# Performance work log

Hardware: AMD Instinct MI355X
Metric: run time of the kernel (lower is better)

The kernel has to match this reference:

```python
import jax, jax.numpy as jnp
import numpy as np
from jax import lax

D_MODEL = 1024
EXPAND = 2
D_INNER = EXPAND * D_MODEL          # 2048
HEADDIM = 64
NHEADS = D_INNER // HEADDIM         # 32
D_STATE = 128
D_CONV = 4
NGROUPS = 1
CONV_DIM = D_INNER + 2 * NGROUPS * D_STATE            # 2304
D_IN_PROJ = 2 * D_INNER + 2 * NGROUPS * D_STATE + NHEADS  # 4384
BATCH, SEQLEN = 2, 2048
EPS = 1e-5


def setup_inputs() -> dict:
    key = jax.random.key(0)
    ks = jax.random.split(key, 10)
    u = jax.random.normal(ks[0], (BATCH, SEQLEN, D_MODEL), jnp.float32)
    W_in = jax.random.normal(ks[1], (D_IN_PROJ, D_MODEL), jnp.float32) * (D_MODEL ** -0.5)
    conv_w = jax.random.normal(ks[2], (CONV_DIM, D_CONV), jnp.float32) * (D_CONV ** -0.5)
    conv_b = jnp.zeros((CONV_DIM,), jnp.float32)
    dt_bias = jnp.log(jnp.exp(jax.random.uniform(ks[3], (NHEADS,), jnp.float32,
                                                 minval=0.001, maxval=0.1)) - 1.0)
    A_log = jnp.log(jax.random.uniform(ks[4], (NHEADS,), jnp.float32, minval=1.0, maxval=16.0))
    D = jnp.ones((NHEADS,), jnp.float32)
    norm_w = jnp.ones((D_INNER,), jnp.float32)
    W_out = jax.random.normal(ks[5], (D_MODEL, D_INNER), jnp.float32) * (D_INNER ** -0.5)
    return {"u": u, "W_in": W_in, "conv_w": conv_w, "conv_b": conv_b,
            "dt_bias": dt_bias, "A_log": A_log, "D": D, "norm_w": norm_w, "W_out": W_out}


def _causal_depthwise_conv(x, w, b):
    # x: [B, L, C], w: [C, K], b: [C]; causal (left) padding K-1
    K = w.shape[1]
    xp = jnp.pad(x, ((0, 0), (K - 1, 0), (0, 0)))
    L = x.shape[1]
    out = b[None, None, :]
    for k in range(K):  # small fixed loop over taps
        out = out + xp[:, k:k + L, :] * w[:, k][None, None, :]
    return out


def _ssd_scan(dt, A, x, Bm, Cm):
    # dt: [B,L,H], A: [H], x: [B,L,H,P], Bm/Cm: [B,L,N]
    Bsz = x.shape[0]
    dA = jnp.exp(dt * A[None, None, :])          # [B,L,H]
    dtx = dt[..., None] * x                       # [B,L,H,P]

    def step(h, inp):
        dA_t, dtx_t, B_t, C_t = inp               # [B,H],[B,H,P],[B,N],[B,N]
        h = h * dA_t[:, :, None, None] + dtx_t[..., None] * B_t[:, None, None, :]
        y = jnp.einsum('bhpn,bn->bhp', h, C_t)
        return h, y

    h0 = jnp.zeros((Bsz, NHEADS, HEADDIM, D_STATE), x.dtype)
    _, ys = lax.scan(step, h0,
                     (dA.transpose(1, 0, 2), dtx.transpose(1, 0, 2, 3),
                      Bm.transpose(1, 0, 2), Cm.transpose(1, 0, 2)))
    return ys.transpose(1, 0, 2, 3)               # [B,L,H,P]


def reference(u, W_in, conv_w, conv_b, dt_bias, A_log, D, norm_w, W_out):
    Bsz, L, _ = u.shape
    zxbcdt = jnp.einsum('bld,ed->ble', u, W_in)                   # [B,L,D_IN_PROJ]
    z = zxbcdt[..., :D_INNER]
    xBC = zxbcdt[..., D_INNER:D_INNER + CONV_DIM]
    dt = zxbcdt[..., D_INNER + CONV_DIM:]                          # [B,L,H]

    xBC = jax.nn.silu(_causal_depthwise_conv(xBC, conv_w, conv_b))
    x = xBC[..., :D_INNER].reshape(Bsz, L, NHEADS, HEADDIM)
    Bm = xBC[..., D_INNER:D_INNER + D_STATE]                       # ngroups=1 -> [B,L,N]
    Cm = xBC[..., D_INNER + D_STATE:]

    dt = jax.nn.softplus(dt + dt_bias[None, None, :])              # [B,L,H]
    A = -jnp.exp(A_log)                                            # [H]

    y = _ssd_scan(dt, A, x, Bm, Cm)                                # [B,L,H,P]
    y = y + D[None, None, :, None] * x
    y = y.reshape(Bsz, L, D_INNER)

    # gated RMSNorm: rmsnorm(y * silu(z)) * weight
    y = y * jax.nn.silu(z)
    y = y * lax.rsqrt(jnp.mean(y * y, axis=-1, keepdims=True) + EPS) * norm_w[None, None, :]

    return jnp.einsum('ble,de->bld', y, W_out)                     # [B,L,D_MODEL]
```

## Files before the change

### kernel.cpp

```cpp
#include <hip/hip_runtime.h>
#include <hip/hip_bf16.h>
#include <math.h>
#include <stdint.h>

#define D_MODEL   1024
#define D_INNER   2048
#define HEADDIM   64
#define NHEADS    32
#define D_STATE   128
#define D_CONV    4
#define CONV_DIM  (D_INNER + 2 * D_STATE)
#define D_IN_PROJ (2 * D_INNER + 2 * D_STATE + NHEADS)
#define N_PAD     4480
#define BATCH     2
#define SEQLEN    2048
#define BL        (BATCH * SEQLEN)
#define EPS       1e-5f

#define NC    16
#define CHUNK 128

typedef __bf16 bf16x8 __attribute__((ext_vector_type(8)));
typedef float  f32x4  __attribute__((ext_vector_type(4)));
typedef unsigned short u16x8 __attribute__((ext_vector_type(8)));

__device__ __forceinline__ float siluf(float x) {
    return x / (1.0f + expf(-x));
}
__device__ __forceinline__ float softplusf(float x) {
    return (x > 20.0f) ? x : log1pf(expf(x));
}
__device__ __forceinline__ unsigned short f2bf(float f) {
    union { float f; unsigned u; } v; v.f = f;
    unsigned r = (v.u + 0x7FFFu + ((v.u >> 16) & 1u)) >> 16;
    return (unsigned short)r;
}

__global__ __launch_bounds__(256) void cast_bf16_kernel(
    const float* __restrict__ in, unsigned short* __restrict__ out, int n8)
{
    const int i = blockIdx.x * 256 + threadIdx.x;
    if (i >= n8) return;
    const float4* p = reinterpret_cast<const float4*>(in + (size_t)i * 8);
    float4 a = p[0], b = p[1];
    u16x8 o;
    o[0] = f2bf(a.x); o[1] = f2bf(a.y); o[2] = f2bf(a.z); o[3] = f2bf(a.w);
    o[4] = f2bf(b.x); o[5] = f2bf(b.y); o[6] = f2bf(b.z); o[7] = f2bf(b.w);
    *reinterpret_cast<u16x8*>(out + (size_t)i * 8) = o;
}

__global__ __launch_bounds__(256) void cast_win_kernel(
    const float* __restrict__ W, unsigned short* __restrict__ out)
{
    const int i = blockIdx.x * 256 + threadIdx.x;
    if (i >= N_PAD * D_MODEL / 8) return;
    const int row = i / (D_MODEL / 8);
    u16x8 o;
    if (row < D_IN_PROJ) {
        const float4* p = reinterpret_cast<const float4*>(W + (size_t)i * 8);
        float4 a = p[0], b = p[1];
        o[0] = f2bf(a.x); o[1] = f2bf(a.y); o[2] = f2bf(a.z); o[3] = f2bf(a.w);
        o[4] = f2bf(b.x); o[5] = f2bf(b.y); o[6] = f2bf(b.z); o[7] = f2bf(b.w);
    } else {
        o = (u16x8)(unsigned short)0;
    }
    *reinterpret_cast<u16x8*>(out + (size_t)i * 8) = o;
}

#define GBM 128
#define GBK 32

__device__ __forceinline__ unsigned swz(unsigned o) {
    return o ^ (((o >> 7) & 7u) << 4);
}

__device__ __forceinline__ void gld_lds16(const unsigned short* gsrc,
                                          unsigned short* lds) {
    auto* l = reinterpret_cast<__attribute__((address_space(3))) unsigned int*>(
        reinterpret_cast<uintptr_t>(lds));
    const auto* g =
        reinterpret_cast<const __attribute__((address_space(1))) unsigned int*>(
            reinterpret_cast<uintptr_t>(gsrc));
    __builtin_amdgcn_global_load_lds(g, l, 16, 0, 0);
}

__global__ __launch_bounds__(256) void gemm_bf16_nt(
    const unsigned short* __restrict__ A, const unsigned short* __restrict__ B,
    float* __restrict__ C, int M, int N, int K, int ldc)
{
    __shared__ unsigned short As[GBM * GBK];
    __shared__ unsigned short Bs[GBM * GBK];

    const int tid = threadIdx.x;
    const int bm = blockIdx.y * GBM;
    const int bn = blockIdx.x * GBM;

    const unsigned d0 = tid * 16;
    const unsigned d1 = 4096 + tid * 16;
    const unsigned o0 = swz(d0), o1 = swz(d1);
    const int r0 = o0 >> 6, c0 = (o0 & 63) >> 1;
    const int r1 = o1 >> 6, c1 = (o1 & 63) >> 1;
    const unsigned short* a_src0 = A + (size_t)(bm + r0) * K + c0;
    const unsigned short* a_src1 = A + (size_t)(bm + r1) * K + c1;
    const unsigned short* b_src0 = B + (size_t)(bn + r0) * K + c0;
    const unsigned short* b_src1 = B + (size_t)(bn + r1) * K + c1;
    unsigned short* a_dst0 = As + (d0 >> 1);
    unsigned short* a_dst1 = As + (d1 >> 1);
    unsigned short* b_dst0 = Bs + (d0 >> 1);
    unsigned short* b_dst1 = Bs + (d1 >> 1);

    const int lane = tid & 63;
    const int wave = tid >> 6;
    const int wr = wave >> 1, wc = wave & 1;
    const int fr = lane & 15;
    const int ko = (lane >> 4) * 8;

    unsigned a_off[4], b_off[4];
    #pragma unroll
    for (int i = 0; i < 4; ++i) {
        a_off[i] = swz(((unsigned)(wr * 64 + i * 16 + fr) << 6) + ko * 2);
        b_off[i] = swz(((unsigned)(wc * 64 + i * 16 + fr) << 6) + ko * 2);
    }

    f32x4 acc[4][4] = {};

    for (int k0 = 0; k0 < K; k0 += GBK) {
        gld_lds16(a_src0, a_dst0);
        gld_lds16(a_src1, a_dst1);
        gld_lds16(b_src0, b_dst0);
        gld_lds16(b_src1, b_dst1);
        __syncthreads();

        bf16x8 af[4], bfr[4];
        #pragma unroll
        for (int i = 0; i < 4; ++i)
            af[i] = *reinterpret_cast<const bf16x8*>(
                reinterpret_cast<const char*>(As) + a_off[i]);
        #pragma unroll
        for (int j = 0; j < 4; ++j)
            bfr[j] = *reinterpret_cast<const bf16x8*>(
                reinterpret_cast<const char*>(Bs) + b_off[j]);
        #pragma unroll
        for (int i = 0; i < 4; ++i)
            #pragma unroll
            for (int j = 0; j < 4; ++j)
                acc[i][j] = __builtin_amdgcn_mfma_f32_16x16x32_bf16(
                    af[i], bfr[j], acc[i][j], 0, 0, 0);
        __syncthreads();
        a_src0 += GBK; a_src1 += GBK; b_src0 += GBK; b_src1 += GBK;
    }

    const int mr = (lane >> 4) * 4;
    #pragma unroll
    for (int i = 0; i < 4; ++i) {
        const int gm = bm + wr * 64 + i * 16 + mr;
        #pragma unroll
        for (int j = 0; j < 4; ++j) {
            const int gn = bn + wc * 64 + j * 16 + fr;
            if (gn < N) {
                #pragma unroll
                for (int r = 0; r < 4; ++r)
                    C[(size_t)(gm + r) * ldc + gn] = acc[i][j][r];
            }
        }
    }
}

__global__ __launch_bounds__(256) void conv_silu_kernel(
    const float* __restrict__ zxbcdt, const float* __restrict__ conv_w,
    const float* __restrict__ conv_b, float* __restrict__ xbc_out)
{
    const int idx = blockIdx.x * 256 + threadIdx.x;
    if (idx >= BL * CONV_DIM) return;
    const int c  = idx % CONV_DIM;
    const int bl = idx / CONV_DIM;
    const int l  = bl % SEQLEN;
    const int b  = bl / SEQLEN;

    float acc = conv_b[c];
    #pragma unroll
    for (int k = 0; k < D_CONV; ++k) {
        const int ll = l + k - (D_CONV - 1);
        if (ll >= 0) {
            acc += zxbcdt[(size_t)(b * SEQLEN + ll) * D_IN_PROJ + D_INNER + c]
                   * conv_w[c * D_CONV + k];
        }
    }
    xbc_out[idx] = siluf(acc);
}

__global__ __launch_bounds__(256) void dt_kernel(
    const float* __restrict__ zxbcdt, const float* __restrict__ dt_bias,
    float* __restrict__ dt_out)
{
    const int idx = blockIdx.x * 256 + threadIdx.x;
    if (idx >= BL * NHEADS) return;
    const int h  = idx % NHEADS;
    const int bl = idx / NHEADS;
    const float v = zxbcdt[(size_t)bl * D_IN_PROJ + D_INNER + CONV_DIM + h]
                    + dt_bias[h];
    dt_out[idx] = softplusf(v);
}

struct LSa { float4 b0, b1, x4; float d; };

__device__ __forceinline__ void load_sa(LSa& L, const float* __restrict__ row,
                                        int xoff, int n0,
                                        const float* __restrict__ dtp, int t) {
    L.b0 = *reinterpret_cast<const float4*>(&row[D_INNER + n0]);
    L.b1 = *reinterpret_cast<const float4*>(&row[D_INNER + n0 + 4]);
    L.x4 = *reinterpret_cast<const float4*>(&row[xoff]);
    L.d  = dtp[(size_t)t * NHEADS];
}

__device__ __forceinline__ void step_sa(float (&hs)[4][8], const LSa& L,
                                        float A_h, float& sdt) {
    sdt += L.d;
    const float dA = __expf(A_h * L.d);
    const float B[8] = {L.b0.x, L.b0.y, L.b0.z, L.b0.w,
                        L.b1.x, L.b1.y, L.b1.z, L.b1.w};
    const float dtx[4] = {L.d * L.x4.x, L.d * L.x4.y, L.d * L.x4.z, L.d * L.x4.w};
    #pragma unroll
    for (int i = 0; i < 4; ++i)
        #pragma unroll
        for (int j = 0; j < 8; ++j)
            hs[i][j] = hs[i][j] * dA + dtx[i] * B[j];
}

__global__ __launch_bounds__(256) void ssd_chunk_state(
    const float* __restrict__ xbc, const float* __restrict__ dt,
    const float* __restrict__ A_log,
    float* __restrict__ S, float* __restrict__ alpha)
{
    const int bid = blockIdx.x;
    const int h = bid & 31;
    const int b = (bid >> 5) & 1;
    const int c = bid >> 6;
    const int tid = threadIdx.x;
    const int pp = tid >> 4;
    const int nc = tid & 15;
    const int n0 = nc * 8;
    const int xoff = h * HEADDIM + pp * 4;

    const float A_h = -__expf(A_log[h]);
    const float* xb  = xbc + (size_t)(b * SEQLEN + c * CHUNK) * CONV_DIM;
    const float* dtp = dt  + (size_t)(b * SEQLEN + c * CHUNK) * NHEADS + h;

    float hs[4][8] = {};
    float sdt = 0.f;
    LSa La, Lb;
    load_sa(La, xb, xoff, n0, dtp, 0);
    for (int t = 0; t < CHUNK; t += 2) {
        load_sa(Lb, xb + (size_t)(t + 1) * CONV_DIM, xoff, n0, dtp, t + 1);
        step_sa(hs, La, A_h, sdt);
        if (t + 2 < CHUNK)
            load_sa(La, xb + (size_t)(t + 2) * CONV_DIM, xoff, n0, dtp, t + 2);
        step_sa(hs, Lb, A_h, sdt);
    }
    const int cbh = (c * 2 + b) * 32 + h;
    float* Sp = S + (size_t)cbh * 8192 + (size_t)(pp * 4) * 128 + n0;
    #pragma unroll
    for (int i = 0; i < 4; ++i) {
        *reinterpret_cast<float4*>(Sp + i * 128) =
            make_float4(hs[i][0], hs[i][1], hs[i][2], hs[i][3]);
        *reinterpret_cast<float4*>(Sp + i * 128 + 4) =
            make_float4(hs[i][4], hs[i][5], hs[i][6], hs[i][7]);
    }
    if (tid == 0) alpha[cbh] = __expf(A_h * sdt);
}

__global__ __launch_bounds__(256) void ssd_state_scan(
    float* __restrict__ S, const float* __restrict__ alpha)
{
    const int bid = blockIdx.x;
    const int q = bid & 3;
    const int h = (bid >> 2) & 31;
    const int b = bid >> 7;
    const int tid = threadIdx.x;
    const size_t off = (size_t)(q * 16 + (tid >> 4)) * 128 + (tid & 15) * 8;
    float h0[8] = {};
    #pragma unroll 2
    for (int c = 0; c < NC; ++c) {
        const int cbh = (c * 2 + b) * 32 + h;
        float* Sp = S + (size_t)cbh * 8192 + off;
        const float al = alpha[cbh];
        float4 t0 = *reinterpret_cast<const float4*>(Sp);
        float4 t1 = *reinterpret_cast<const float4*>(Sp + 4);
        *reinterpret_cast<float4*>(Sp)     = make_float4(h0[0], h0[1], h0[2], h0[3]);
        *reinterpret_cast<float4*>(Sp + 4) = make_float4(h0[4], h0[5], h0[6], h0[7]);
        h0[0] = h0[0] * al + t0.x;
        h0[1] = h0[1] * al + t0.y;
        h0[2] = h0[2] * al + t0.z;
        h0[3] = h0[3] * al + t0.w;
        h0[4] = h0[4] * al + t1.x;
        h0[5] = h0[5] * al + t1.y;
        h0[6] = h0[6] * al + t1.z;
        h0[7] = h0[7] * al + t1.w;
    }
}

struct LSc { float4 b0, b1, c0, c1, x4; float d; };

__device__ __forceinline__ void load_sc(LSc& L, const float* __restrict__ row,
                                        int xoff, int n0,
                                        const float* __restrict__ dtp, int t) {
    L.b0 = *reinterpret_cast<const float4*>(&row[D_INNER + n0]);
    L.b1 = *reinterpret_cast<const float4*>(&row[D_INNER + n0 + 4]);
    L.c0 = *reinterpret_cast<const float4*>(&row[D_INNER + D_STATE + n0]);
    L.c1 = *reinterpret_cast<const float4*>(&row[D_INNER + D_STATE + n0 + 4]);
    L.x4 = *reinterpret_cast<const float4*>(&row[xoff]);
    L.d  = dtp[(size_t)t * NHEADS];
}

__device__ __forceinline__ void step_sc(float (&hs)[4][8], const LSc& L,
                                        float A_h, float (&acc)[4]) {
    const float dA = __expf(A_h * L.d);
    const float B[8] = {L.b0.x, L.b0.y, L.b0.z, L.b0.w,
                        L.b1.x, L.b1.y, L.b1.z, L.b1.w};
    const float C[8] = {L.c0.x, L.c0.y, L.c0.z, L.c0.w,
                        L.c1.x, L.c1.y, L.c1.z, L.c1.w};
    const float dtx[4] = {L.d * L.x4.x, L.d * L.x4.y, L.d * L.x4.z, L.d * L.x4.w};
    #pragma unroll
    for (int i = 0; i < 4; ++i) {
        float a = 0.f;
        #pragma unroll
        for (int j = 0; j < 8; ++j) {
            hs[i][j] = hs[i][j] * dA + dtx[i] * B[j];
            a += hs[i][j] * C[j];
        }
        acc[i] = a;
    }
}

__device__ __forceinline__ void reduce_store(float (&acc)[4], const LSc& L,
                                             float D_h, int nc, float* dst) {
    #pragma unroll
    for (int i = 0; i < 4; ++i) {
        acc[i] += __shfl_xor(acc[i], 1, 64);
        acc[i] += __shfl_xor(acc[i], 2, 64);
        acc[i] += __shfl_xor(acc[i], 4, 64);
        acc[i] += __shfl_xor(acc[i], 8, 64);
    }
    if (nc == 0) {
        float4 o;
        o.x = acc[0] + D_h * L.x4.x;
        o.y = acc[1] + D_h * L.x4.y;
        o.z = acc[2] + D_h * L.x4.z;
        o.w = acc[3] + D_h * L.x4.w;
        *reinterpret_cast<float4*>(dst) = o;
    }
}

__global__ __launch_bounds__(256) void ssd_chunk_out(
    const float* __restrict__ xbc, const float* __restrict__ dt,
    const float* __restrict__ A_log, const float* __restrict__ Dp,
    const float* __restrict__ S, float* __restrict__ y)
{
    const int bid = blockIdx.x;
    const int h = bid & 31;
    const int b = (bid >> 5) & 1;
    const int c = bid >> 6;
    const int tid = threadIdx.x;
    const int pp = tid >> 4;
    const int nc = tid & 15;
    const int n0 = nc * 8;
    const int xoff = h * HEADDIM + pp * 4;

    const float A_h = -__expf(A_log[h]);
    const float D_h = Dp[h];
    const float* xb  = xbc + (size_t)(b * SEQLEN + c * CHUNK) * CONV_DIM;
    const float* dtp = dt  + (size_t)(b * SEQLEN + c * CHUNK) * NHEADS + h;
    float* yb = y + (size_t)(b * SEQLEN + c * CHUNK) * D_INNER + xoff;

    const int cbh = (c * 2 + b) * 32 + h;
    float hs[4][8];
    {
        const float* Hp = S + (size_t)cbh * 8192 + (size_t)(pp * 4) * 128 + n0;
        #pragma unroll
        for (int i = 0; i < 4; ++i) {
            float4 h0 = *reinterpret_cast<const float4*>(Hp + i * 128);
            float4 h1 = *reinterpret_cast<const float4*>(Hp + i * 128 + 4);
            hs[i][0] = h0.x; hs[i][1] = h0.y; hs[i][2] = h0.z; hs[i][3] = h0.w;
            hs[i][4] = h1.x; hs[i][5] = h1.y; hs[i][6] = h1.z; hs[i][7] = h1.w;
        }
    }

    LSc La, Lb;
    load_sc(La, xb, xoff, n0, dtp, 0);
    for (int t = 0; t < CHUNK; t += 2) {
        load_sc(Lb, xb + (size_t)(t + 1) * CONV_DIM, xoff, n0, dtp, t + 1);
        float acc[4];
        step_sc(hs, La, A_h, acc);
        reduce_store(acc, La, D_h, nc, yb + (size_t)t * D_INNER);
        if (t + 2 < CHUNK)
            load_sc(La, xb + (size_t)(t + 2) * CONV_DIM, xoff, n0, dtp, t + 2);
        float acc2[4];
        step_sc(hs, Lb, A_h, acc2);
        reduce_store(acc2, Lb, D_h, nc, yb + (size_t)(t + 1) * D_INNER);
    }
}

__global__ __launch_bounds__(256) void gate_norm_kernel(
    const float* __restrict__ y,
    const float* __restrict__ zxbcdt,
    const float* __restrict__ norm_w,
    unsigned short* __restrict__ ybf)
{
    const int row = blockIdx.x;
    const int tid = threadIdx.x;
    const float* yr = y + (size_t)row * D_INNER;
    const float* zr = zxbcdt + (size_t)row * D_IN_PROJ;

    float v[8];
    float ss = 0.f;
    #pragma unroll
    for (int j = 0; j < 2; ++j) {
        float4 y4 = *reinterpret_cast<const float4*>(&yr[tid * 8 + j * 4]);
        float4 z4 = *reinterpret_cast<const float4*>(&zr[tid * 8 + j * 4]);
        float a0 = y4.x * siluf(z4.x);
        float a1 = y4.y * siluf(z4.y);
        float a2 = y4.z * siluf(z4.z);
        float a3 = y4.w * siluf(z4.w);
        v[j * 4 + 0] = a0; v[j * 4 + 1] = a1;
        v[j * 4 + 2] = a2; v[j * 4 + 3] = a3;
        ss += a0 * a0 + a1 * a1 + a2 * a2 + a3 * a3;
    }
    #pragma unroll
    for (int o = 1; o < 64; o <<= 1) ss += __shfl_xor(ss, o, 64);
    __shared__ float red[4];
    if ((tid & 63) == 0) red[tid >> 6] = ss;
    __syncthreads();
    const float tot = red[0] + red[1] + red[2] + red[3];
    const float rs = rsqrtf(tot * (1.0f / D_INNER) + EPS);

    const float4* nw = reinterpret_cast<const float4*>(&norm_w[tid * 8]);
    float4 w0 = nw[0], w1 = nw[1];
    u16x8 o;
    o[0] = f2bf(v[0] * rs * w0.x);
    o[1] = f2bf(v[1] * rs * w0.y);
    o[2] = f2bf(v[2] * rs * w0.z);
    o[3] = f2bf(v[3] * rs * w0.w);
    o[4] = f2bf(v[4] * rs * w1.x);
    o[5] = f2bf(v[5] * rs * w1.y);
    o[6] = f2bf(v[6] * rs * w1.z);
    o[7] = f2bf(v[7] * rs * w1.w);
    *reinterpret_cast<u16x8*>(&ybf[(size_t)row * D_INNER + tid * 8]) = o;
}

extern "C" void kernel_launch(void* const* d_in, const int* in_sizes, int n_in,
                              void* d_out, int out_size, void* d_ws, size_t ws_size,
                              hipStream_t stream)
{
    const float* u       = (const float*)d_in[0];
    const float* W_in    = (const float*)d_in[1];
    const float* conv_w  = (const float*)d_in[2];
    const float* conv_b  = (const float*)d_in[3];
    const float* dt_bias = (const float*)d_in[4];
    const float* A_log   = (const float*)d_in[5];
    const float* Dp      = (const float*)d_in[6];
    const float* norm_w  = (const float*)d_in[7];
    const float* W_out   = (const float*)d_in[8];
    float* out = (float*)d_out;

    float* zxbcdt = (float*)d_ws;
    float* xbc    = zxbcdt + (size_t)BL * D_IN_PROJ;
    float* dt_sp  = xbc    + (size_t)BL * CONV_DIM;
    float* yb     = dt_sp  + (size_t)BL * NHEADS;
    float* Sbuf   = yb     + (size_t)BL * D_INNER;
    float* alphab = Sbuf   + (size_t)NC * BATCH * NHEADS * HEADDIM * D_STATE;

    unsigned short* ubf  = (unsigned short*)Sbuf;
    unsigned short* wibf = (unsigned short*)Sbuf + (size_t)BL * D_MODEL;
    unsigned short* ybbf = (unsigned short*)Sbuf;
    unsigned short* wobf = (unsigned short*)Sbuf + (size_t)BL * D_INNER;

    cast_bf16_kernel<<<(BL * D_MODEL / 8 + 255) / 256, 256, 0, stream>>>(
        u, ubf, BL * D_MODEL / 8);
    cast_win_kernel<<<(N_PAD * D_MODEL / 8 + 255) / 256, 256, 0, stream>>>(
        W_in, wibf);
    {
        dim3 grid(N_PAD / GBM, BL / GBM);
        gemm_bf16_nt<<<grid, 256, 0, stream>>>(
            ubf, wibf, zxbcdt, BL, D_IN_PROJ, D_MODEL, D_IN_PROJ);
    }
    {
        const int n = BL * CONV_DIM;
        conv_silu_kernel<<<(n + 255) / 256, 256, 0, stream>>>(
            zxbcdt, conv_w, conv_b, xbc);
    }
    {
        const int n = BL * NHEADS;
        dt_kernel<<<(n + 255) / 256, 256, 0, stream>>>(zxbcdt, dt_bias, dt_sp);
    }
    ssd_chunk_state<<<NC * BATCH * NHEADS, 256, 0, stream>>>(
        xbc, dt_sp, A_log, Sbuf, alphab);
    ssd_state_scan<<<BATCH * NHEADS * 4, 256, 0, stream>>>(Sbuf, alphab);
    ssd_chunk_out<<<NC * BATCH * NHEADS, 256, 0, stream>>>(
        xbc, dt_sp, A_log, Dp, Sbuf, yb);
    cast_bf16_kernel<<<(D_MODEL * D_INNER / 8 + 255) / 256, 256, 0, stream>>>(
        W_out, wobf, D_MODEL * D_INNER / 8);
    gate_norm_kernel<<<BL, 256, 0, stream>>>(yb, zxbcdt, norm_w, ybbf);
    {
        dim3 grid(D_MODEL / GBM, BL / GBM);
        gemm_bf16_nt<<<grid, 256, 0, stream>>>(
            ybbf, wobf, out, BL, D_MODEL, D_INNER, D_MODEL);
    }
}
```

Before: 494.6 us.

## Rewrite chunk output scan as SSD matmul form using bf16 MFMA

Replaces the sequential per-timestep recurrence in the chunk output kernel with the chunked SSD formulation. It computes C·Bᵀ, applies the causal decay mask from cumulative dt·A, multiplies by dt·x, and adds the inter-chunk term C·H scaled by the decay, all with bf16 MFMA in LDS. The D skip term moves into the gate-norm kernel. This removes the serial 128-step loop and its shuffle reductions per step, at the cost of bf16 rounding of B, C, x and state, and about 96KB of LDS per block, which limits occupancy.

```diff
diff --git a/kernel.cpp b/kernel.cpp
--- a/kernel.cpp
+++ b/kernel.cpp
@@ -23,6 +23,7 @@
 typedef __bf16 bf16x8 __attribute__((ext_vector_type(8)));
 typedef float  f32x4  __attribute__((ext_vector_type(4)));
 typedef unsigned short u16x8 __attribute__((ext_vector_type(8)));
+typedef unsigned short u16x4 __attribute__((ext_vector_type(4)));
 
 __device__ __forceinline__ float siluf(float x) {
     return x / (1.0f + expf(-x));
@@ -72,6 +73,9 @@
 
 __device__ __forceinline__ unsigned swz(unsigned o) {
     return o ^ (((o >> 7) & 7u) << 4);
+}
+__device__ __forceinline__ unsigned swz256(unsigned o) {
+    return o ^ (((o >> 8) & 7u) << 4);
 }
 
 __device__ __forceinline__ void gld_lds16(const unsigned short* gsrc,
@@ -299,110 +303,196 @@
     }
 }
 
-struct LSc { float4 b0, b1, c0, c1, x4; float d; };
-
-__device__ __forceinline__ void load_sc(LSc& L, const float* __restrict__ row,
-                                        int xoff, int n0,
-                                        const float* __restrict__ dtp, int t) {
-    L.b0 = *reinterpret_cast<const float4*>(&row[D_INNER + n0]);
-    L.b1 = *reinterpret_cast<const float4*>(&row[D_INNER + n0 + 4]);
-    L.c0 = *reinterpret_cast<const float4*>(&row[D_INNER + D_STATE + n0]);
-    L.c1 = *reinterpret_cast<const float4*>(&row[D_INNER + D_STATE + n0 + 4]);
-    L.x4 = *reinterpret_cast<const float4*>(&row[xoff]);
-    L.d  = dtp[(size_t)t * NHEADS];
-}
-
-__device__ __forceinline__ void step_sc(float (&hs)[4][8], const LSc& L,
-                                        float A_h, float (&acc)[4]) {
-    const float dA = __expf(A_h * L.d);
-    const float B[8] = {L.b0.x, L.b0.y, L.b0.z, L.b0.w,
-                        L.b1.x, L.b1.y, L.b1.z, L.b1.w};
-    const float C[8] = {L.c0.x, L.c0.y, L.c0.z, L.c0.w,
-                        L.c1.x, L.c1.y, L.c1.z, L.c1.w};
-    const float dtx[4] = {L.d * L.x4.x, L.d * L.x4.y, L.d * L.x4.z, L.d * L.x4.w};
-    #pragma unroll
-    for (int i = 0; i < 4; ++i) {
-        float a = 0.f;
-        #pragma unroll
-        for (int j = 0; j < 8; ++j) {
-            hs[i][j] = hs[i][j] * dA + dtx[i] * B[j];
-            a += hs[i][j] * C[j];
-        }
-        acc[i] = a;
-    }
-}
-
-__device__ __forceinline__ void reduce_store(float (&acc)[4], const LSc& L,
-                                             float D_h, int nc, float* dst) {
-    #pragma unroll
-    for (int i = 0; i < 4; ++i) {
-        acc[i] += __shfl_xor(acc[i], 1, 64);
-        acc[i] += __shfl_xor(acc[i], 2, 64);
-        acc[i] += __shfl_xor(acc[i], 4, 64);
-        acc[i] += __shfl_xor(acc[i], 8, 64);
-    }
-    if (nc == 0) {
-        float4 o;
-        o.x = acc[0] + D_h * L.x4.x;
-        o.y = acc[1] + D_h * L.x4.y;
-        o.z = acc[2] + D_h * L.x4.z;
-        o.w = acc[3] + D_h * L.x4.w;
-        *reinterpret_cast<float4*>(dst) = o;
-    }
-}
-
-__global__ __launch_bounds__(256) void ssd_chunk_out(
+__global__ __launch_bounds__(256) void ssd_chunk_out_mfma(
     const float* __restrict__ xbc, const float* __restrict__ dt,
-    const float* __restrict__ A_log, const float* __restrict__ Dp,
-    const float* __restrict__ S, float* __restrict__ y)
-{
+    const float* __restrict__ A_log, const float* __restrict__ S,
+    float* __restrict__ y)
+{
+    __shared__ __align__(16) unsigned char sm[98824];
+    constexpr unsigned OB = 0;
+    constexpr unsigned OC = 32768;
+    constexpr unsigned OX = 65536;
+    constexpr unsigned OH = 81920;
+    constexpr unsigned OL = 98304;
+    constexpr unsigned OW = 98816;
+
     const int bid = blockIdx.x;
     const int h = bid & 31;
     const int b = (bid >> 5) & 1;
     const int c = bid >> 6;
     const int tid = threadIdx.x;
-    const int pp = tid >> 4;
-    const int nc = tid & 15;
-    const int n0 = nc * 8;
-    const int xoff = h * HEADDIM + pp * 4;
+    const int lane = tid & 63;
+    const int wave = tid >> 6;
+
+    float* lcf  = reinterpret_cast<float*>(sm + OL);
+    float* wtot = reinterpret_cast<float*>(sm + OW);
 
     const float A_h = -__expf(A_log[h]);
-    const float D_h = Dp[h];
-    const float* xb  = xbc + (size_t)(b * SEQLEN + c * CHUNK) * CONV_DIM;
-    const float* dtp = dt  + (size_t)(b * SEQLEN + c * CHUNK) * NHEADS + h;
-    float* yb = y + (size_t)(b * SEQLEN + c * CHUNK) * D_INNER + xoff;
-
-    const int cbh = (c * 2 + b) * 32 + h;
-    float hs[4][8];
+    const int row0 = b * SEQLEN + c * CHUNK;
+    const float* dtp = dt + (size_t)row0 * NHEADS + h;
+
+    float sv = 0.f;
+    if (tid < 128) {
+        sv = dtp[(size_t)tid * NHEADS];
+        #pragma unroll
+        for (int o = 1; o < 64; o <<= 1) {
+            float u = __shfl_up(sv, o, 64);
+            if ((tid & 63) >= o) sv += u;
+        }
+    }
+    if (tid == 63) *wtot = sv;
+    __syncthreads();
+    if (tid < 128) {
+        const float tot = (tid >= 64) ? *wtot : 0.f;
+        lcf[tid] = A_h * (sv + tot);
+    }
+
     {
-        const float* Hp = S + (size_t)cbh * 8192 + (size_t)(pp * 4) * 128 + n0;
-        #pragma unroll
-        for (int i = 0; i < 4; ++i) {
-            float4 h0 = *reinterpret_cast<const float4*>(Hp + i * 128);
-            float4 h1 = *reinterpret_cast<const float4*>(Hp + i * 128 + 4);
-            hs[i][0] = h0.x; hs[i][1] = h0.y; hs[i][2] = h0.z; hs[i][3] = h0.w;
-            hs[i][4] = h1.x; hs[i][5] = h1.y; hs[i][6] = h1.z; hs[i][7] = h1.w;
-        }
-    }
-
-    LSc La, Lb;
-    load_sc(La, xb, xoff, n0, dtp, 0);
-    for (int t = 0; t < CHUNK; t += 2) {
-        load_sc(Lb, xb + (size_t)(t + 1) * CONV_DIM, xoff, n0, dtp, t + 1);
-        float acc[4];
-        step_sc(hs, La, A_h, acc);
-        reduce_store(acc, La, D_h, nc, yb + (size_t)t * D_INNER);
-        if (t + 2 < CHUNK)
-            load_sc(La, xb + (size_t)(t + 2) * CONV_DIM, xoff, n0, dtp, t + 2);
-        float acc2[4];
-        step_sc(hs, Lb, A_h, acc2);
-        reduce_store(acc2, Lb, D_h, nc, yb + (size_t)(t + 1) * D_INNER);
+        const int r = tid >> 1, half = tid & 1;
+        const float* rowB = xbc + (size_t)(row0 + r) * CONV_DIM + D_INNER + half * 64;
+        const float* rowC = rowB + D_STATE;
+        #pragma unroll
+        for (int j = 0; j < 16; ++j) {
+            float4 vb = reinterpret_cast<const float4*>(rowB)[j];
+            float4 vc = reinterpret_cast<const float4*>(rowC)[j];
+            const unsigned o8 = (unsigned)r * 256 + half * 128 + j * 8;
+            u16x4 wb = {f2bf(vb.x), f2bf(vb.y), f2bf(vb.z), f2bf(vb.w)};
+            u16x4 wc = {f2bf(vc.x), f2bf(vc.y), f2bf(vc.z), f2bf(vc.w)};
+            *reinterpret_cast<u16x4*>(sm + OB + swz256(o8)) = wb;
+            *reinterpret_cast<u16x4*>(sm + OC + swz256(o8)) = wc;
+        }
+    }
+    {
+        const int s = tid >> 1, ph = (tid & 1) * 32;
+        const float dts = dtp[(size_t)s * NHEADS];
+        const float* rowX = xbc + (size_t)(row0 + s) * CONV_DIM + h * HEADDIM + ph;
+        #pragma unroll
+        for (int j = 0; j < 8; ++j) {
+            float4 v = reinterpret_cast<const float4*>(rowX)[j];
+            const int p0 = ph + j * 4;
+            *reinterpret_cast<unsigned short*>(sm + OX + swz256((unsigned)(p0 + 0) * 256 + s * 2)) = f2bf(v.x * dts);
+            *reinterpret_cast<unsigned short*>(sm + OX + swz256((unsigned)(p0 + 1) * 256 + s * 2)) = f2bf(v.y * dts);
+            *reinterpret_cast<unsigned short*>(sm + OX + swz256((unsigned)(p0 + 2) * 256 + s * 2)) = f2bf(v.z * dts);
+            *reinterpret_cast<unsigned short*>(sm + OX + swz256((unsigned)(p0 + 3) * 256 + s * 2)) = f2bf(v.w * dts);
+        }
+    }
+    {
+        const int cbh = (c * 2 + b) * 32 + h;
+        const float* Hp = S + (size_t)cbh * 8192 + tid * 32;
+        #pragma unroll
+        for (int j = 0; j < 8; ++j) {
+            float4 v = reinterpret_cast<const float4*>(Hp)[j];
+            const unsigned o8 = (unsigned)tid * 64 + j * 8;
+            u16x4 w = {f2bf(v.x), f2bf(v.y), f2bf(v.z), f2bf(v.w)};
+            *reinterpret_cast<u16x4*>(sm + OH + swz256(o8)) = w;
+        }
+    }
+    __syncthreads();
+
+    const int fr  = lane & 15;
+    const int ko2 = (lane >> 4) * 16;
+    const int g   = lane >> 4;
+
+    const int wr = wave >> 1, wc = wave & 1;
+    f32x4 sacc[4][4] = {};
+    #pragma unroll
+    for (int ks = 0; ks < 4; ++ks) {
+        bf16x8 cf[4], bf[4];
+        #pragma unroll
+        for (int i = 0; i < 4; ++i)
+            cf[i] = *reinterpret_cast<const bf16x8*>(sm + OC +
+                swz256((unsigned)(wr * 64 + i * 16 + fr) * 256 + ks * 64 + ko2));
+        #pragma unroll
+        for (int j = 0; j < 4; ++j)
+            bf[j] = *reinterpret_cast<const bf16x8*>(sm + OB +
+                swz256((unsigned)(wc * 64 + j * 16 + fr) * 256 + ks * 64 + ko2));
+        #pragma unroll
+        for (int i = 0; i < 4; ++i)
+            #pragma unroll
+            for (int j = 0; j < 4; ++j)
+                sacc[i][j] = __builtin_amdgcn_mfma_f32_16x16x32_bf16(
+                    cf[i], bf[j], sacc[i][j], 0, 0, 0);
+    }
+
+    const int tw = wave * 32;
+    f32x4 acc2[2][4] = {};
+    #pragma unroll
+    for (int kn = 0; kn < 4; ++kn) {
+        bf16x8 ca[2], hv[4];
+        #pragma unroll
+        for (int i = 0; i < 2; ++i)
+            ca[i] = *reinterpret_cast<const bf16x8*>(sm + OC +
+                swz256((unsigned)(tw + i * 16 + fr) * 256 + kn * 64 + ko2));
+        #pragma unroll
+        for (int j = 0; j < 4; ++j)
+            hv[j] = *reinterpret_cast<const bf16x8*>(sm + OH +
+                swz256((unsigned)(j * 16 + fr) * 256 + kn * 64 + ko2));
+        #pragma unroll
+        for (int i = 0; i < 2; ++i)
+            #pragma unroll
+            for (int j = 0; j < 4; ++j)
+                acc2[i][j] = __builtin_amdgcn_mfma_f32_16x16x32_bf16(
+                    ca[i], hv[j], acc2[i][j], 0, 0, 0);
+    }
+    __syncthreads();
+
+    #pragma unroll
+    for (int i = 0; i < 4; ++i) {
+        #pragma unroll
+        for (int r = 0; r < 4; ++r) {
+            const int t = wr * 64 + i * 16 + g * 4 + r;
+            const float lct = lcf[t];
+            #pragma unroll
+            for (int j = 0; j < 4; ++j) {
+                const int s = wc * 64 + j * 16 + fr;
+                float pv = 0.f;
+                if (s <= t) pv = sacc[i][j][r] * __expf(lct - lcf[s]);
+                *reinterpret_cast<unsigned short*>(
+                    sm + OC + swz256((unsigned)t * 256 + s * 2)) = f2bf(pv);
+            }
+        }
+    }
+    __syncthreads();
+
+    f32x4 acc1[2][4] = {};
+    #pragma unroll
+    for (int ks = 0; ks < 4; ++ks) {
+        bf16x8 pa[2], xv[4];
+        #pragma unroll
+        for (int i = 0; i < 2; ++i)
+            pa[i] = *reinterpret_cast<const bf16x8*>(sm + OC +
+                swz256((unsigned)(tw + i * 16 + fr) * 256 + ks * 64 + ko2));
+        #pragma unroll
+        for (int j = 0; j < 4; ++j)
+            xv[j] = *reinterpret_cast<const bf16x8*>(sm + OX +
+                swz256((unsigned)(j * 16 + fr) * 256 + ks * 64 + ko2));
+        #pragma unroll
+        for (int i = 0; i < 2; ++i)
+            #pragma unroll
+            for (int j = 0; j < 4; ++j)
+                acc1[i][j] = __builtin_amdgcn_mfma_f32_16x16x32_bf16(
+                    pa[i], xv[j], acc1[i][j], 0, 0, 0);
+    }
+
+    #pragma unroll
+    for (int i = 0; i < 2; ++i) {
+        #pragma unroll
+        for (int r = 0; r < 4; ++r) {
+            const int t = tw + i * 16 + g * 4 + r;
+            const float el = __expf(lcf[t]);
+            float* yrow = y + (size_t)(row0 + t) * D_INNER + h * HEADDIM;
+            #pragma unroll
+            for (int j = 0; j < 4; ++j)
+                yrow[j * 16 + fr] = acc1[i][j][r] + el * acc2[i][j][r];
+        }
     }
 }
 
 __global__ __launch_bounds__(256) void gate_norm_kernel(
     const float* __restrict__ y,
     const float* __restrict__ zxbcdt,
+    const float* __restrict__ xbc,
+    const float* __restrict__ Dp,
     const float* __restrict__ norm_w,
     unsigned short* __restrict__ ybf)
 {
@@ -410,6 +500,8 @@
     const int tid = threadIdx.x;
     const float* yr = y + (size_t)row * D_INNER;
     const float* zr = zxbcdt + (size_t)row * D_IN_PROJ;
+    const float* xr = xbc + (size_t)row * CONV_DIM;
+    const float Dh = Dp[tid >> 3];
 
     float v[8];
     float ss = 0.f;
@@ -417,10 +509,11 @@
     for (int j = 0; j < 2; ++j) {
         float4 y4 = *reinterpret_cast<const float4*>(&yr[tid * 8 + j * 4]);
         float4 z4 = *reinterpret_cast<const float4*>(&zr[tid * 8 + j * 4]);
-        float a0 = y4.x * siluf(z4.x);
-        float a1 = y4.y * siluf(z4.y);
-        float a2 = y4.z * siluf(z4.z);
-        float a3 = y4.w * siluf(z4.w);
+        float4 x4 = *reinterpret_cast<const float4*>(&xr[tid * 8 + j * 4]);
+        float a0 = (y4.x + Dh * x4.x) * siluf(z4.x);
+        float a1 = (y4.y + Dh * x4.y) * siluf(z4.y);
+        float a2 = (y4.z + Dh * x4.z) * siluf(z4.z);
+        float a3 = (y4.w + Dh * x4.w) * siluf(z4.w);
         v[j * 4 + 0] = a0; v[j * 4 + 1] = a1;
         v[j * 4 + 2] = a2; v[j * 4 + 3] = a3;
         ss += a0 * a0 + a1 * a1 + a2 * a2 + a3 * a3;
@@ -495,11 +588,11 @@
     ssd_chunk_state<<<NC * BATCH * NHEADS, 256, 0, stream>>>(
         xbc, dt_sp, A_log, Sbuf, alphab);
     ssd_state_scan<<<BATCH * NHEADS * 4, 256, 0, stream>>>(Sbuf, alphab);
-    ssd_chunk_out<<<NC * BATCH * NHEADS, 256, 0, stream>>>(
-        xbc, dt_sp, A_log, Dp, Sbuf, yb);
+    ssd_chunk_out_mfma<<<NC * BATCH * NHEADS, 256, 0, stream>>>(
+        xbc, dt_sp, A_log, Sbuf, yb);
     cast_bf16_kernel<<<(D_MODEL * D_INNER / 8 + 255) / 256, 256, 0, stream>>>(
         W_out, wobf, D_MODEL * D_INNER / 8);
-    gate_norm_kernel<<<BL, 256, 0, stream>>>(yb, zxbcdt, norm_w, ybbf);
+    gate_norm_kernel<<<BL, 256, 0, stream>>>(yb, zxbcdt, xbc, Dp, norm_w, ybbf);
     {
         dim3 grid(D_MODEL / GBM, BL / GBM);
         gemm_bf16_nt<<<grid, 256, 0, stream>>>(
```

New measurement: 434.9 us. -12.1%, faster.
